# Performance work log

Hardware: AMD Instinct MI355X
Metric: run time of the kernel (lower is better)

Reference implementation:

```python
import jax, jax.numpy as jnp
import numpy as np

B, L, V, D = 8, 1024, 64, 64  # num_vars == d_model required by the module's g*h broadcast
EPS = 1e-5


def _layer_norm(x, gamma, beta):
    mu = jnp.mean(x, axis=-1, keepdims=True)
    var = jnp.mean(jnp.square(x - mu), axis=-1, keepdims=True)
    return (x - mu) * jax.lax.rsqrt(var + EPS) * gamma + beta


def setup_inputs() -> dict:
    key = jax.random.key(0)
    ks = jax.random.split(key, 20)
    s = 0.05
    inp = {
        'x': jax.random.normal(ks[0], (B, L, V), jnp.float32),
        # per-variable GRN(1, D, D) params, batched over V
        'W1': jax.random.normal(ks[1], (V, D), jnp.float32) * s,   # lin1 weight [in=1 -> D]
        'b1': jax.random.normal(ks[2], (V, D), jnp.float32) * s,
        'W2': jax.random.normal(ks[3], (V, D, D), jnp.float32) * s,
        'b2': jax.random.normal(ks[4], (V, D), jnp.float32) * s,
        'Wg': jax.random.normal(ks[5], (V, D, D), jnp.float32) * s,
        'bg': jax.random.normal(ks[6], (V, D), jnp.float32) * s,
        'Wsk': jax.random.normal(ks[7], (V, D), jnp.float32) * s,  # skip Linear(1, D)
        'bsk': jax.random.normal(ks[8], (V, D), jnp.float32) * s,
        'gamma': jnp.ones((V, D), jnp.float32),
        'beta': jnp.zeros((V, D), jnp.float32),
        # weight_net GRN(V*D, D, V) params
        'Wn1': jax.random.normal(ks[9], (V * D, D), jnp.float32) * s,
        'bn1': jax.random.normal(ks[10], (D,), jnp.float32) * s,
        'Wn2': jax.random.normal(ks[11], (D, D), jnp.float32) * s,
        'bn2': jax.random.normal(ks[12], (D,), jnp.float32) * s,
        'Wng': jax.random.normal(ks[13], (D, V), jnp.float32) * s,
        'bng': jax.random.normal(ks[14], (V,), jnp.float32) * s,
        'Wns': jax.random.normal(ks[15], (V * D, V), jnp.float32) * s,
        'bns': jax.random.normal(ks[16], (V,), jnp.float32) * s,
        'ngamma': jnp.ones((V,), jnp.float32),
        'nbeta': jnp.zeros((V,), jnp.float32),
    }
    return inp


def reference(x, W1, b1, W2, b2, Wg, bg, Wsk, bsk, gamma, beta,
              Wn1, bn1, Wn2, bn2, Wng, bng, Wns, bns, ngamma, nbeta):
    Bx, Lx, Vx = x.shape
    # --- per-variable GRN(1, D, D), batched over the variable axis ---
    h1 = jax.nn.elu(x[..., None] * W1 + b1)                      # [B,L,V,D]
    h2 = jnp.einsum('blvd,vde->blve', h1, W2) + b2               # [B,L,V,D]
    g = jax.nn.sigmoid(jnp.einsum('blvd,vde->blve', h2, Wg) + bg)
    skip = x[..., None] * Wsk + bsk                              # [B,L,V,D]
    stacked = _layer_norm(skip + g * h2, gamma, beta)            # [B,L,V,D]
    # --- weight net GRN(V*D, D, V) + softmax (note: requires V == D) ---
    flat = stacked.reshape(Bx, Lx, Vx * stacked.shape[-1])
    hw = jax.nn.elu(flat @ Wn1 + bn1)                            # [B,L,D]
    hw = hw @ Wn2 + bn2                                          # [B,L,D]
    gw = jax.nn.sigmoid(hw @ Wng + bng)                          # [B,L,V]
    skw = flat @ Wns + bns                                       # [B,L,V]
    weights = jax.nn.softmax(_layer_norm(skw + gw * hw, ngamma, nbeta), axis=-1)
    return jnp.einsum('blv,blvd->bld', weights, stacked)
```

## Files before the change

### kernel.cpp

```cpp
#include <hip/hip_runtime.h>
#include <hip/hip_bf16.h>
#include <math.h>

#define NV 64
#define ND 64
#define NTOK 8192
#define LN_EPS 1e-5f
#define SROW 4096
#define WROW 4096
#define KSPLIT 8
#define KR2 (4096 / KSPLIT)
#define BK 64
#define PROW2 (KSPLIT * 128)

typedef __attribute__((ext_vector_type(8))) short s8v;
typedef __attribute__((ext_vector_type(4))) float f4v;
typedef __attribute__((ext_vector_type(4))) int   i4v;

__device__ __forceinline__ float sigm_f(float x) {
    return __builtin_amdgcn_rcpf(1.f + __expf(-x));
}
__device__ __forceinline__ float elu_f(float x)  { return x > 0.f ? x : (__expf(x) - 1.f); }

__device__ __forceinline__ float bf16_to_f(unsigned short s) {
    union { unsigned int u; float f; } c; c.u = ((unsigned int)s) << 16;
    return c.f;
}
__device__ __forceinline__ unsigned short bf16_rn(float f) {
    union { float f; unsigned int u; } c; c.f = f;
    return (unsigned short)((c.u + 0x8000u) >> 16);
}

__global__ __launch_bounds__(256) void vsn_prepack(
    const float* __restrict__ W2, const float* __restrict__ Wg,
    const float* __restrict__ Wn1, const float* __restrict__ Wns,
    short* __restrict__ w2b, short* __restrict__ wgb,
    short* __restrict__ wct)
{
    __shared__ float T[64][65];
    const int b = blockIdx.x, t = threadIdx.x;

    if (b < 64) {
        const float* src = W2 + (size_t)b * 4096;
        short* dst = w2b + (size_t)b * 4096;
        #pragma unroll
        for (int pass = 0; pass < 2; ++pass) {
            #pragma unroll
            for (int i = 0; i < 16; ++i) {
                int id = i * 256 + t;
                T[id & 63][id >> 6] = src[id];
            }
            __syncthreads();
            #pragma unroll
            for (int i = 0; i < 16; ++i) {
                int id = i * 256 + t;
                dst[id] = (short)bf16_rn(T[id >> 6][id & 63]);
            }
            __syncthreads();
            src = Wg + (size_t)b * 4096;
            dst = wgb + (size_t)b * 4096;
        }
    } else {
        int tb = b - 64;
        int half = tb >> 6, kt = tb & 63;
        const float* src = (half == 0 ? Wn1 : Wns) + (size_t)(kt * 64) * 64;
        #pragma unroll
        for (int i = 0; i < 16; ++i) {
            int id = i * 256 + t;
            T[id & 63][id >> 6] = src[id];
        }
        __syncthreads();
        #pragma unroll
        for (int i = 0; i < 16; ++i) {
            int id = i * 256 + t;
            int n = id >> 6, r = id & 63;
            wct[(size_t)(half * 64 + n) * WROW + kt * 64 + r] = (short)bf16_rn(T[n][r]);
        }
    }
}

__global__ __launch_bounds__(256) void vsn_stage1(
    const float* __restrict__ x,
    const float* __restrict__ W1, const float* __restrict__ b1,
    const short* __restrict__ w2b, const short* __restrict__ wgb,
    const float* __restrict__ b2, const float* __restrict__ bg,
    const float* __restrict__ Wsk, const float* __restrict__ bsk,
    const float* __restrict__ gamma, const float* __restrict__ beta,
    unsigned short* __restrict__ stb)
{
    const int t = threadIdx.x;
    const int wave = t >> 6, lane = t & 63;
    const int m16 = lane & 15, quad = lane >> 4;
    const int v = blockIdx.y * 4 + wave;

    __shared__ float xs[4][32];
    __shared__ __align__(16) unsigned short h2s[4][32][72];

    float w1k[2][8], b1k[2][8];
    #pragma unroll
    for (int kt = 0; kt < 2; ++kt) {
        *(float4*)&w1k[kt][0] = *(const float4*)(W1 + v * 64 + kt * 32 + quad * 8);
        *(float4*)&w1k[kt][4] = *(const float4*)(W1 + v * 64 + kt * 32 + quad * 8 + 4);
        *(float4*)&b1k[kt][0] = *(const float4*)(b1 + v * 64 + kt * 32 + quad * 8);
        *(float4*)&b1k[kt][4] = *(const float4*)(b1 + v * 64 + kt * 32 + quad * 8 + 4);
    }
    float b2d[4], bgd[4], wskd[4], bskd[4], gamd[4], betd[4];
    #pragma unroll
    for (int ni = 0; ni < 4; ++ni) {
        int d = v * 64 + ni * 16 + m16;
        b2d[ni] = b2[d]; bgd[ni] = bg[d]; wskd[ni] = Wsk[d]; bskd[ni] = bsk[d];
        gamd[ni] = gamma[d]; betd[ni] = beta[d];
    }
    const size_t wb = (size_t)v * 4096;

    for (int tt4 = 0; tt4 < 4; ++tt4) {
        const int tile0 = blockIdx.x * 128 + tt4 * 32;

        if (lane < 32) xs[wave][lane] = x[(size_t)(tile0 + lane) * NV + v];

        s8v a[2][2];
        #pragma unroll
        for (int kt = 0; kt < 2; ++kt)
            #pragma unroll
            for (int mi = 0; mi < 2; ++mi) {
                float xv = xs[wave][mi * 16 + m16];
                float h[8];
                #pragma unroll
                for (int j = 0; j < 8; ++j) h[j] = elu_f(fmaf(xv, w1k[kt][j], b1k[kt][j]));
                i4v av;
                #pragma unroll
                for (int p = 0; p < 4; ++p) {
                    unsigned int u0 = __float_as_uint(h[2 * p]);
                    unsigned int u1 = __float_as_uint(h[2 * p + 1]);
                    av[p] = (int)((u1 & 0xffff0000u) | (u0 >> 16));
                }
                a[mi][kt] = *(s8v*)&av;
            }

        f4v hacc[2][4];
        #pragma unroll
        for (int mi = 0; mi < 2; ++mi)
            #pragma unroll
            for (int ni = 0; ni < 4; ++ni) hacc[mi][ni] = (f4v){0.f, 0.f, 0.f, 0.f};
        #pragma unroll
        for (int ni = 0; ni < 4; ++ni)
            #pragma unroll
            for (int kt = 0; kt < 2; ++kt) {
                s8v bh = *(const s8v*)(w2b + wb + (size_t)(ni * 16 + m16) * 64 + kt * 32 + quad * 8);
                #pragma unroll
                for (int mi = 0; mi < 2; ++mi)
                    hacc[mi][ni] = __builtin_amdgcn_mfma_f32_16x16x32_bf16(a[mi][kt], bh, hacc[mi][ni], 0, 0, 0);
            }
        #pragma unroll
        for (int mi = 0; mi < 2; ++mi)
            #pragma unroll
            for (int ni = 0; ni < 4; ++ni)
                #pragma unroll
                for (int r = 0; r < 4; ++r) hacc[mi][ni][r] += b2d[ni];

        #pragma unroll
        for (int mi = 0; mi < 2; ++mi)
            #pragma unroll
            for (int ni = 0; ni < 4; ++ni)
                #pragma unroll
                for (int r = 0; r < 4; ++r)
                    h2s[wave][mi * 16 + quad * 4 + r][ni * 16 + m16] =
                        (unsigned short)(__float_as_uint(hacc[mi][ni][r]) >> 16);

        s8v c[2][2];
        #pragma unroll
        for (int mi = 0; mi < 2; ++mi)
            #pragma unroll
            for (int kt = 0; kt < 2; ++kt)
                c[mi][kt] = *(const s8v*)&h2s[wave][mi * 16 + m16][kt * 32 + quad * 8];

        f4v gacc[2][4];
        #pragma unroll
        for (int mi = 0; mi < 2; ++mi)
            #pragma unroll
            for (int ni = 0; ni < 4; ++ni) gacc[mi][ni] = (f4v){0.f, 0.f, 0.f, 0.f};
        #pragma unroll
        for (int ni = 0; ni < 4; ++ni)
            #pragma unroll
            for (int kt = 0; kt < 2; ++kt) {
                s8v bh = *(const s8v*)(wgb + wb + (size_t)(ni * 16 + m16) * 64 + kt * 32 + quad * 8);
                #pragma unroll
                for (int mi = 0; mi < 2; ++mi)
                    gacc[mi][ni] = __builtin_amdgcn_mfma_f32_16x16x32_bf16(c[mi][kt], bh, gacc[mi][ni], 0, 0, 0);
            }

        {
            float xtok[2][4];
            #pragma unroll
            for (int mi = 0; mi < 2; ++mi)
                #pragma unroll
                for (int r = 0; r < 4; ++r) xtok[mi][r] = xs[wave][mi * 16 + quad * 4 + r];
            #pragma unroll
            for (int mi = 0; mi < 2; ++mi)
                #pragma unroll
                for (int ni = 0; ni < 4; ++ni)
                    #pragma unroll
                    for (int r = 0; r < 4; ++r) {
                        float g = sigm_f(gacc[mi][ni][r] + bgd[ni]);
                        gacc[mi][ni][r] = fmaf(xtok[mi][r], wskd[ni], bskd[ni]) + g * hacc[mi][ni][r];
                    }
        }

        #pragma unroll
        for (int mi = 0; mi < 2; ++mi)
            #pragma unroll
            for (int r = 0; r < 4; ++r) {
                float s0 = gacc[mi][0][r], s1 = gacc[mi][1][r], s2 = gacc[mi][2][r], s3 = gacc[mi][3][r];
                float sum = s0 + s1 + s2 + s3;
                float sq  = s0 * s0 + s1 * s1 + s2 * s2 + s3 * s3;
                #pragma unroll
                for (int m = 1; m < 16; m <<= 1) { sum += __shfl_xor(sum, m); sq += __shfl_xor(sq, m); }
                float mu  = sum * 0.015625f;
                float var = sq * 0.015625f - mu * mu;
                float rs  = __builtin_amdgcn_rsqf(var + LN_EPS);
                size_t base = (size_t)(tile0 + mi * 16 + quad * 4 + r) * SROW + (size_t)v * 64 + m16;
                #pragma unroll
                for (int ni = 0; ni < 4; ++ni)
                    stb[base + ni * 16] =
                        bf16_rn((gacc[mi][ni][r] - mu) * rs * gamd[ni] + betd[ni]);
            }
    }
}

__global__ __launch_bounds__(512) void vsn_stage2a(
    const unsigned short* __restrict__ stb,
    const short* __restrict__ wct,
    float* __restrict__ part)
{
    const int t = threadIdx.x;
    const int wave = t >> 6, lane = t & 63;
    const int m16 = lane & 15, quad = lane >> 4;
    const int mw = wave & 3, nw = wave >> 2;
    const int tok0 = blockIdx.x * 128;
    const int s = blockIdx.y;
    const int k0 = s * KR2;

    __shared__ __align__(16) unsigned short Al[128][72];
    __shared__ __align__(16) unsigned short Bl[128][72];

    const int srow = t >> 3;
    const int scol = (t & 7) * 8;
    const short* A = (const short*)stb;

    f4v acc[2][4];
    #pragma unroll
    for (int mi = 0; mi < 2; ++mi)
        #pragma unroll
        for (int nj = 0; nj < 4; ++nj) acc[mi][nj] = (f4v){0.f, 0.f, 0.f, 0.f};

    s8v pa[2], pb[2];
    #pragma unroll
    for (int q = 0; q < 2; ++q) {
        int row = srow + q * 64;
        pa[q] = *(const s8v*)(A + (size_t)(tok0 + row) * SROW + k0 + scol);
        pb[q] = *(const s8v*)(wct + (size_t)row * WROW + k0 + scol);
    }

    for (int kc = 0; kc < KR2 / BK; ++kc) {
        if (kc > 0) __syncthreads();
        #pragma unroll
        for (int q = 0; q < 2; ++q) {
            int row = srow + q * 64;
            *(s8v*)&Al[row][scol] = pa[q];
            *(s8v*)&Bl[row][scol] = pb[q];
        }
        __syncthreads();
        if (kc + 1 < KR2 / BK) {
            int kn = k0 + (kc + 1) * BK;
            #pragma unroll
            for (int q = 0; q < 2; ++q) {
                int row = srow + q * 64;
                pa[q] = *(const s8v*)(A + (size_t)(tok0 + row) * SROW + kn + scol);
                pb[q] = *(const s8v*)(wct + (size_t)row * WROW + kn + scol);
            }
        }
        #pragma unroll
        for (int ks = 0; ks < 2; ++ks) {
            s8v af[2], bf[4];
            #pragma unroll
            for (int mi = 0; mi < 2; ++mi)
                af[mi] = *(const s8v*)&Al[mw * 32 + mi * 16 + m16][ks * 32 + quad * 8];
            #pragma unroll
            for (int nj = 0; nj < 4; ++nj)
                bf[nj] = *(const s8v*)&Bl[nw * 64 + nj * 16 + m16][ks * 32 + quad * 8];
            #pragma unroll
            for (int mi = 0; mi < 2; ++mi)
                #pragma unroll
                for (int nj = 0; nj < 4; ++nj)
                    acc[mi][nj] = __builtin_amdgcn_mfma_f32_16x16x32_bf16(af[mi], bf[nj], acc[mi][nj], 0, 0, 0);
        }
    }

    #pragma unroll
    for (int mi = 0; mi < 2; ++mi)
        #pragma unroll
        for (int nj = 0; nj < 4; ++nj)
            #pragma unroll
            for (int r = 0; r < 4; ++r)
                part[(size_t)(tok0 + mw * 32 + mi * 16 + quad * 4 + r) * PROW2
                     + s * 128 + nw * 64 + nj * 16 + m16] = acc[mi][nj][r];
}

__global__ __launch_bounds__(256) void vsn_stage2b(
    const unsigned short* __restrict__ stb, const float* __restrict__ part,
    const float* __restrict__ bn1,
    const float* __restrict__ Wn2, const float* __restrict__ bn2,
    const float* __restrict__ Wng, const float* __restrict__ bng,
    const float* __restrict__ bns,
    const float* __restrict__ ngamma, const float* __restrict__ nbeta,
    float* __restrict__ out)
{
    const int t = threadIdx.x;
    const int tok0 = blockIdx.x * 8;
    const int lane = t & 63, wv = t >> 6;

    __shared__ __align__(16) float hw1_s[8][64];
    __shared__ __align__(16) float skw_s[8][64];
    __shared__ __align__(16) float hw2_s[8][64];
    __shared__ float s2_s[8][64];
    __shared__ float w_s[8][64];

    #pragma unroll
    for (int tk = 0; tk < 2; ++tk) {
        int tl = wv * 2 + tk;
        const float* pr = part + (size_t)(tok0 + tl) * PROW2
                        + (lane >> 5) * 128 + (lane & 31) * 4;
        float tv[4] = {0.f, 0.f, 0.f, 0.f};
        #pragma unroll
        for (int i = 0; i < 4; ++i) {
            float4 a = *(const float4*)(pr + i * 256);
            tv[0] += a.x; tv[1] += a.y; tv[2] += a.z; tv[3] += a.w;
        }
        #pragma unroll
        for (int c = 0; c < 4; ++c) tv[c] += __shfl_xor(tv[c], 32);
        if (lane < 16) {
            int j0 = lane * 4;
            float4 bb = *(const float4*)(bn1 + j0);
            hw1_s[tl][j0 + 0] = elu_f(tv[0] + bb.x);
            hw1_s[tl][j0 + 1] = elu_f(tv[1] + bb.y);
            hw1_s[tl][j0 + 2] = elu_f(tv[2] + bb.z);
            hw1_s[tl][j0 + 3] = elu_f(tv[3] + bb.w);
        } else if (lane < 32) {
            int j0 = (lane - 16) * 4;
            float4 bb = *(const float4*)(bns + j0);
            skw_s[tl][j0 + 0] = tv[0] + bb.x;
            skw_s[tl][j0 + 1] = tv[1] + bb.y;
            skw_s[tl][j0 + 2] = tv[2] + bb.z;
            skw_s[tl][j0 + 3] = tv[3] + bb.w;
        }
    }
    __syncthreads();

    #pragma unroll
    for (int i = 0; i < 2; ++i) {
        int oidx = i * 256 + t;
        int tt = oidx >> 6, jj = oidx & 63;
        float acc = bn2[jj];
        #pragma unroll
        for (int k4 = 0; k4 < 16; ++k4) {
            float4 h = *(const float4*)&hw1_s[tt][k4 * 4];
            acc += h.x * Wn2[(k4*4+0)*64+jj] + h.y * Wn2[(k4*4+1)*64+jj]
                 + h.z * Wn2[(k4*4+2)*64+jj] + h.w * Wn2[(k4*4+3)*64+jj];
        }
        hw2_s[tt][jj] = acc;
    }
    __syncthreads();

    #pragma unroll
    for (int i = 0; i < 2; ++i) {
        int oidx = i * 256 + t;
        int tt = oidx >> 6, vv = oidx & 63;
        float acc = bng[vv];
        #pragma unroll
        for (int k4 = 0; k4 < 16; ++k4) {
            float4 h = *(const float4*)&hw2_s[tt][k4 * 4];
            acc += h.x * Wng[(k4*4+0)*64+vv] + h.y * Wng[(k4*4+1)*64+vv]
                 + h.z * Wng[(k4*4+2)*64+vv] + h.w * Wng[(k4*4+3)*64+vv];
        }
        float gw = sigm_f(acc);
        s2_s[tt][vv] = skw_s[tt][vv] + gw * hw2_s[tt][vv];
    }
    __syncthreads();

    const int vloc = lane >> 3, d8 = (lane & 7) * 8;
    s8v r0[8], r1[8];
    {
        const short* s0 = (const short*)stb + (size_t)(tok0 + wv * 2) * SROW + d8;
        const short* s1 = s0 + SROW;
        #pragma unroll
        for (int vc = 0; vc < 8; ++vc) {
            r0[vc] = *(const s8v*)(s0 + (vc * 8 + vloc) * 64);
            r1[vc] = *(const s8v*)(s1 + (vc * 8 + vloc) * 64);
        }
    }

    if (t < 128) {
        int tt = t >> 4, l = t & 15;
        float z[4]; float sum = 0.f, sq = 0.f;
        #pragma unroll
        for (int i = 0; i < 4; ++i) { z[i] = s2_s[tt][l + 16 * i]; sum += z[i]; sq += z[i] * z[i]; }
        #pragma unroll
        for (int m = 1; m < 16; m <<= 1) { sum += __shfl_xor(sum, m); sq += __shfl_xor(sq, m); }
        float mu  = sum * 0.015625f;
        float var = sq * 0.015625f - mu * mu;
        float rs  = __builtin_amdgcn_rsqf(var + LN_EPS);
        float ln[4]; float mx = -1e30f;
        #pragma unroll
        for (int i = 0; i < 4; ++i) {
            ln[i] = (z[i] - mu) * rs * ngamma[l + 16 * i] + nbeta[l + 16 * i];
            mx = fmaxf(mx, ln[i]);
        }
        #pragma unroll
        for (int m = 1; m < 16; m <<= 1) mx = fmaxf(mx, __shfl_xor(mx, m));
        float es = 0.f; float ev[4];
        #pragma unroll
        for (int i = 0; i < 4; ++i) { ev[i] = __expf(ln[i] - mx); es += ev[i]; }
        #pragma unroll
        for (int m = 1; m < 16; m <<= 1) es += __shfl_xor(es, m);
        float inv = __builtin_amdgcn_rcpf(es);
        #pragma unroll
        for (int i = 0; i < 4; ++i) w_s[tt][l + 16 * i] = ev[i] * inv;
    }
    __syncthreads();

    {
        float acc0[8], acc1[8];
        #pragma unroll
        for (int j = 0; j < 8; ++j) { acc0[j] = 0.f; acc1[j] = 0.f; }
        #pragma unroll
        for (int vc = 0; vc < 8; ++vc) {
            int v = vc * 8 + vloc;
            float w0 = w_s[wv * 2][v], w1 = w_s[wv * 2 + 1][v];
            #pragma unroll
            for (int j = 0; j < 8; ++j) {
                acc0[j] = fmaf(w0, bf16_to_f((unsigned short)r0[vc][j]), acc0[j]);
                acc1[j] = fmaf(w1, bf16_to_f((unsigned short)r1[vc][j]), acc1[j]);
            }
        }
        #pragma unroll
        for (int m = 8; m <= 32; m <<= 1)
            #pragma unroll
            for (int j = 0; j < 8; ++j) {
                acc0[j] += __shfl_xor(acc0[j], m);
                acc1[j] += __shfl_xor(acc1[j], m);
            }
        if (lane < 8) {
            float* op = out + (size_t)(tok0 + wv * 2) * 64 + lane * 8;
            *(float4*)op       = make_float4(acc0[0], acc0[1], acc0[2], acc0[3]);
            *(float4*)(op + 4) = make_float4(acc0[4], acc0[5], acc0[6], acc0[7]);
            op += 64;
            *(float4*)op       = make_float4(acc1[0], acc1[1], acc1[2], acc1[3]);
            *(float4*)(op + 4) = make_float4(acc1[4], acc1[5], acc1[6], acc1[7]);
        }
    }
}

extern "C" void kernel_launch(void* const* d_in, const int* in_sizes, int n_in,
                              void* d_out, int out_size, void* d_ws, size_t ws_size,
                              hipStream_t stream) {
    const float* x     = (const float*)d_in[0];
    const float* W1    = (const float*)d_in[1];
    const float* b1    = (const float*)d_in[2];
    const float* W2    = (const float*)d_in[3];
    const float* b2    = (const float*)d_in[4];
    const float* Wg    = (const float*)d_in[5];
    const float* bg    = (const float*)d_in[6];
    const float* Wsk   = (const float*)d_in[7];
    const float* bsk   = (const float*)d_in[8];
    const float* gamma = (const float*)d_in[9];
    const float* beta  = (const float*)d_in[10];
    const float* Wn1   = (const float*)d_in[11];
    const float* bn1   = (const float*)d_in[12];
    const float* Wn2   = (const float*)d_in[13];
    const float* bn2   = (const float*)d_in[14];
    const float* Wng   = (const float*)d_in[15];
    const float* bng   = (const float*)d_in[16];
    const float* Wns   = (const float*)d_in[17];
    const float* bns   = (const float*)d_in[18];
    const float* ngam  = (const float*)d_in[19];
    const float* nbet  = (const float*)d_in[20];

    char* ws = (char*)d_ws;
    unsigned short* stb = (unsigned short*)ws;
    short* wct = (short*)(ws + (64u << 20));
    short* w2b = (short*)(ws + (65u << 20));
    short* wgb = w2b + 262144;
    float* part = (float*)(ws + (66u << 20));
    float* outp = (float*)d_out;

    vsn_prepack<<<dim3(192), 256, 0, stream>>>(W2, Wg, Wn1, Wns, w2b, wgb, wct);
    vsn_stage1<<<dim3(NTOK / 128, 16), 256, 0, stream>>>(
        x, W1, b1, w2b, wgb, b2, bg, Wsk, bsk, gamma, beta, stb);
    vsn_stage2a<<<dim3(NTOK / 128, KSPLIT), 512, 0, stream>>>(stb, wct, part);
    vsn_stage2b<<<dim3(NTOK / 8), 256, 0, stream>>>(
        stb, part, bn1, Wn2, bn2, Wng, bng, bns, ngam, nbet, outp);
}
```

Before: 186.3 us.

## Transpose stage1 MFMA orientation for packed stores; async LDS loads with swizzle in stage2a

Stage1 swaps the MFMA operand roles so each lane holds four consecutive feature values per token. This turns the scalar bf16 stores of the normalized output and the h2 staging writes into packed 64-bit stores, and moves the per-feature params into shared memory. Stage2a replaces register-staged loads with global_load_lds async copies into double-buffered, XOR-swizzled LDS tiles. That removes padding and register staging in exchange for relying on the direct-to-LDS load path and its lane-to-address mapping being correct.

```diff
diff --git a/kernel.cpp b/kernel.cpp
--- a/kernel.cpp
+++ b/kernel.cpp
@@ -11,6 +11,7 @@
 #define KSPLIT 8
 #define KR2 (4096 / KSPLIT)
 #define BK 64
+#define NKC (KR2 / BK)
 #define PROW2 (KSPLIT * 128)
 
 typedef __attribute__((ext_vector_type(8))) short s8v;
@@ -29,6 +30,18 @@
 __device__ __forceinline__ unsigned short bf16_rn(float f) {
     union { float f; unsigned int u; } c; c.f = f;
     return (unsigned short)((c.u + 0x8000u) >> 16);
+}
+__device__ __forceinline__ unsigned int pk2rn(float a, float b) {
+    return (unsigned int)bf16_rn(a) | ((unsigned int)bf16_rn(b) << 16);
+}
+__device__ __forceinline__ unsigned int pk2t(float a, float b) {
+    return (__float_as_uint(a) >> 16) | (__float_as_uint(b) & 0xffff0000u);
+}
+__device__ __forceinline__ void async16(const void* g, void* l) {
+    __builtin_amdgcn_global_load_lds(
+        (const __attribute__((address_space(1))) unsigned int*)g,
+        (__attribute__((address_space(3))) unsigned int*)l,
+        16, 0, 0);
 }
 
 __global__ __launch_bounds__(256) void vsn_prepack(
@@ -93,8 +106,18 @@
     const int m16 = lane & 15, quad = lane >> 4;
     const int v = blockIdx.y * 4 + wave;
 
-    __shared__ float xs[4][32];
     __shared__ __align__(16) unsigned short h2s[4][32][72];
+    __shared__ __align__(16) float pl[4][6][64];
+
+    {
+        int dd = lane;
+        pl[wave][0][dd] = b2[v * 64 + dd];
+        pl[wave][1][dd] = bg[v * 64 + dd];
+        pl[wave][2][dd] = Wsk[v * 64 + dd];
+        pl[wave][3][dd] = bsk[v * 64 + dd];
+        pl[wave][4][dd] = gamma[v * 64 + dd];
+        pl[wave][5][dd] = beta[v * 64 + dd];
+    }
 
     float w1k[2][8], b1k[2][8];
     #pragma unroll
@@ -104,126 +127,131 @@
         *(float4*)&b1k[kt][0] = *(const float4*)(b1 + v * 64 + kt * 32 + quad * 8);
         *(float4*)&b1k[kt][4] = *(const float4*)(b1 + v * 64 + kt * 32 + quad * 8 + 4);
     }
-    float b2d[4], bgd[4], wskd[4], bskd[4], gamd[4], betd[4];
-    #pragma unroll
-    for (int ni = 0; ni < 4; ++ni) {
-        int d = v * 64 + ni * 16 + m16;
-        b2d[ni] = b2[d]; bgd[ni] = bg[d]; wskd[ni] = Wsk[d]; bskd[ni] = bsk[d];
-        gamd[ni] = gamma[d]; betd[ni] = beta[d];
-    }
     const size_t wb = (size_t)v * 4096;
 
     for (int tt4 = 0; tt4 < 4; ++tt4) {
         const int tile0 = blockIdx.x * 128 + tt4 * 32;
 
-        if (lane < 32) xs[wave][lane] = x[(size_t)(tile0 + lane) * NV + v];
-
-        s8v a[2][2];
+        float xld = x[(size_t)(tile0 + (lane & 31)) * NV + v];
+        float xv[2];
+        xv[0] = __shfl(xld, m16);
+        xv[1] = __shfl(xld, 16 + m16);
+
+        s8v bh1[2][2];
+        #pragma unroll
+        for (int ti = 0; ti < 2; ++ti)
+            #pragma unroll
+            for (int kt = 0; kt < 2; ++kt) {
+                float h[8];
+                #pragma unroll
+                for (int j = 0; j < 8; ++j) h[j] = elu_f(fmaf(xv[ti], w1k[kt][j], b1k[kt][j]));
+                i4v av;
+                #pragma unroll
+                for (int p = 0; p < 4; ++p)
+                    av[p] = (int)pk2t(h[2 * p], h[2 * p + 1]);
+                bh1[ti][kt] = *(s8v*)&av;
+            }
+
+        f4v hacc[4][2];
+        #pragma unroll
+        for (int ei = 0; ei < 4; ++ei)
+            #pragma unroll
+            for (int ti = 0; ti < 2; ++ti) hacc[ei][ti] = (f4v){0.f, 0.f, 0.f, 0.f};
         #pragma unroll
         for (int kt = 0; kt < 2; ++kt)
             #pragma unroll
-            for (int mi = 0; mi < 2; ++mi) {
-                float xv = xs[wave][mi * 16 + m16];
-                float h[8];
-                #pragma unroll
-                for (int j = 0; j < 8; ++j) h[j] = elu_f(fmaf(xv, w1k[kt][j], b1k[kt][j]));
-                i4v av;
-                #pragma unroll
-                for (int p = 0; p < 4; ++p) {
-                    unsigned int u0 = __float_as_uint(h[2 * p]);
-                    unsigned int u1 = __float_as_uint(h[2 * p + 1]);
-                    av[p] = (int)((u1 & 0xffff0000u) | (u0 >> 16));
+            for (int ei = 0; ei < 4; ++ei) {
+                s8v aw = *(const s8v*)(w2b + wb + (size_t)(ei * 16 + m16) * 64 + kt * 32 + quad * 8);
+                #pragma unroll
+                for (int ti = 0; ti < 2; ++ti)
+                    hacc[ei][ti] = __builtin_amdgcn_mfma_f32_16x16x32_bf16(aw, bh1[ti][kt], hacc[ei][ti], 0, 0, 0);
+            }
+
+        #pragma unroll
+        for (int ei = 0; ei < 4; ++ei) {
+            float bq[4];
+            *(float4*)bq = *(const float4*)&pl[wave][0][ei * 16 + quad * 4];
+            #pragma unroll
+            for (int ti = 0; ti < 2; ++ti) {
+                #pragma unroll
+                for (int r = 0; r < 4; ++r) hacc[ei][ti][r] += bq[r];
+                uint2 pk = make_uint2(pk2t(hacc[ei][ti][0], hacc[ei][ti][1]),
+                                      pk2t(hacc[ei][ti][2], hacc[ei][ti][3]));
+                *(uint2*)&h2s[wave][ti * 16 + m16][ei * 16 + quad * 4] = pk;
+            }
+        }
+
+        s8v bh2[2][2];
+        #pragma unroll
+        for (int ti = 0; ti < 2; ++ti)
+            #pragma unroll
+            for (int kt = 0; kt < 2; ++kt)
+                bh2[ti][kt] = *(const s8v*)&h2s[wave][ti * 16 + m16][kt * 32 + quad * 8];
+
+        f4v gacc[4][2];
+        #pragma unroll
+        for (int ei = 0; ei < 4; ++ei)
+            #pragma unroll
+            for (int ti = 0; ti < 2; ++ti) gacc[ei][ti] = (f4v){0.f, 0.f, 0.f, 0.f};
+        #pragma unroll
+        for (int kt = 0; kt < 2; ++kt)
+            #pragma unroll
+            for (int ei = 0; ei < 4; ++ei) {
+                s8v ag = *(const s8v*)(wgb + wb + (size_t)(ei * 16 + m16) * 64 + kt * 32 + quad * 8);
+                #pragma unroll
+                for (int ti = 0; ti < 2; ++ti)
+                    gacc[ei][ti] = __builtin_amdgcn_mfma_f32_16x16x32_bf16(ag, bh2[ti][kt], gacc[ei][ti], 0, 0, 0);
+            }
+
+        #pragma unroll
+        for (int ei = 0; ei < 4; ++ei) {
+            float bgq[4], wkq[4], bkq[4];
+            *(float4*)bgq = *(const float4*)&pl[wave][1][ei * 16 + quad * 4];
+            *(float4*)wkq = *(const float4*)&pl[wave][2][ei * 16 + quad * 4];
+            *(float4*)bkq = *(const float4*)&pl[wave][3][ei * 16 + quad * 4];
+            #pragma unroll
+            for (int ti = 0; ti < 2; ++ti)
+                #pragma unroll
+                for (int r = 0; r < 4; ++r) {
+                    float g = sigm_f(gacc[ei][ti][r] + bgq[r]);
+                    gacc[ei][ti][r] = fmaf(xv[ti], wkq[r], bkq[r]) + g * hacc[ei][ti][r];
                 }
-                a[mi][kt] = *(s8v*)&av;
-            }
-
-        f4v hacc[2][4];
-        #pragma unroll
-        for (int mi = 0; mi < 2; ++mi)
-            #pragma unroll
-            for (int ni = 0; ni < 4; ++ni) hacc[mi][ni] = (f4v){0.f, 0.f, 0.f, 0.f};
-        #pragma unroll
-        for (int ni = 0; ni < 4; ++ni)
-            #pragma unroll
-            for (int kt = 0; kt < 2; ++kt) {
-                s8v bh = *(const s8v*)(w2b + wb + (size_t)(ni * 16 + m16) * 64 + kt * 32 + quad * 8);
-                #pragma unroll
-                for (int mi = 0; mi < 2; ++mi)
-                    hacc[mi][ni] = __builtin_amdgcn_mfma_f32_16x16x32_bf16(a[mi][kt], bh, hacc[mi][ni], 0, 0, 0);
-            }
-        #pragma unroll
-        for (int mi = 0; mi < 2; ++mi)
-            #pragma unroll
-            for (int ni = 0; ni < 4; ++ni)
-                #pragma unroll
-                for (int r = 0; r < 4; ++r) hacc[mi][ni][r] += b2d[ni];
-
-        #pragma unroll
-        for (int mi = 0; mi < 2; ++mi)
-            #pragma unroll
-            for (int ni = 0; ni < 4; ++ni)
-                #pragma unroll
-                for (int r = 0; r < 4; ++r)
-                    h2s[wave][mi * 16 + quad * 4 + r][ni * 16 + m16] =
-                        (unsigned short)(__float_as_uint(hacc[mi][ni][r]) >> 16);
-
-        s8v c[2][2];
-        #pragma unroll
-        for (int mi = 0; mi < 2; ++mi)
-            #pragma unroll
-            for (int kt = 0; kt < 2; ++kt)
-                c[mi][kt] = *(const s8v*)&h2s[wave][mi * 16 + m16][kt * 32 + quad * 8];
-
-        f4v gacc[2][4];
-        #pragma unroll
-        for (int mi = 0; mi < 2; ++mi)
-            #pragma unroll
-            for (int ni = 0; ni < 4; ++ni) gacc[mi][ni] = (f4v){0.f, 0.f, 0.f, 0.f};
-        #pragma unroll
-        for (int ni = 0; ni < 4; ++ni)
-            #pragma unroll
-            for (int kt = 0; kt < 2; ++kt) {
-                s8v bh = *(const s8v*)(wgb + wb + (size_t)(ni * 16 + m16) * 64 + kt * 32 + quad * 8);
-                #pragma unroll
-                for (int mi = 0; mi < 2; ++mi)
-                    gacc[mi][ni] = __builtin_amdgcn_mfma_f32_16x16x32_bf16(c[mi][kt], bh, gacc[mi][ni], 0, 0, 0);
-            }
-
-        {
-            float xtok[2][4];
-            #pragma unroll
-            for (int mi = 0; mi < 2; ++mi)
-                #pragma unroll
-                for (int r = 0; r < 4; ++r) xtok[mi][r] = xs[wave][mi * 16 + quad * 4 + r];
-            #pragma unroll
-            for (int mi = 0; mi < 2; ++mi)
-                #pragma unroll
-                for (int ni = 0; ni < 4; ++ni)
-                    #pragma unroll
-                    for (int r = 0; r < 4; ++r) {
-                        float g = sigm_f(gacc[mi][ni][r] + bgd[ni]);
-                        gacc[mi][ni][r] = fmaf(xtok[mi][r], wskd[ni], bskd[ni]) + g * hacc[mi][ni][r];
-                    }
-        }
-
-        #pragma unroll
-        for (int mi = 0; mi < 2; ++mi)
-            #pragma unroll
-            for (int r = 0; r < 4; ++r) {
-                float s0 = gacc[mi][0][r], s1 = gacc[mi][1][r], s2 = gacc[mi][2][r], s3 = gacc[mi][3][r];
-                float sum = s0 + s1 + s2 + s3;
-                float sq  = s0 * s0 + s1 * s1 + s2 * s2 + s3 * s3;
-                #pragma unroll
-                for (int m = 1; m < 16; m <<= 1) { sum += __shfl_xor(sum, m); sq += __shfl_xor(sq, m); }
-                float mu  = sum * 0.015625f;
-                float var = sq * 0.015625f - mu * mu;
-                float rs  = __builtin_amdgcn_rsqf(var + LN_EPS);
-                size_t base = (size_t)(tile0 + mi * 16 + quad * 4 + r) * SROW + (size_t)v * 64 + m16;
-                #pragma unroll
-                for (int ni = 0; ni < 4; ++ni)
-                    stb[base + ni * 16] =
-                        bf16_rn((gacc[mi][ni][r] - mu) * rs * gamd[ni] + betd[ni]);
-            }
+        }
+
+        float mu[2], rs[2];
+        #pragma unroll
+        for (int ti = 0; ti < 2; ++ti) {
+            float sum = 0.f, sq = 0.f;
+            #pragma unroll
+            for (int ei = 0; ei < 4; ++ei)
+                #pragma unroll
+                for (int r = 0; r < 4; ++r) {
+                    float z = gacc[ei][ti][r];
+                    sum += z; sq = fmaf(z, z, sq);
+                }
+            sum += __shfl_xor(sum, 16); sq += __shfl_xor(sq, 16);
+            sum += __shfl_xor(sum, 32); sq += __shfl_xor(sq, 32);
+            mu[ti] = sum * 0.015625f;
+            float var = sq * 0.015625f - mu[ti] * mu[ti];
+            rs[ti] = __builtin_amdgcn_rsqf(var + LN_EPS);
+        }
+
+        #pragma unroll
+        for (int ei = 0; ei < 4; ++ei) {
+            float gq[4], bq[4];
+            *(float4*)gq = *(const float4*)&pl[wave][4][ei * 16 + quad * 4];
+            *(float4*)bq = *(const float4*)&pl[wave][5][ei * 16 + quad * 4];
+            #pragma unroll
+            for (int ti = 0; ti < 2; ++ti) {
+                float n0 = (gacc[ei][ti][0] - mu[ti]) * rs[ti] * gq[0] + bq[0];
+                float n1 = (gacc[ei][ti][1] - mu[ti]) * rs[ti] * gq[1] + bq[1];
+                float n2 = (gacc[ei][ti][2] - mu[ti]) * rs[ti] * gq[2] + bq[2];
+                float n3 = (gacc[ei][ti][3] - mu[ti]) * rs[ti] * gq[3] + bq[3];
+                uint2 pk = make_uint2(pk2rn(n0, n1), pk2rn(n2, n3));
+                *(uint2*)(stb + (size_t)(tile0 + ti * 16 + m16) * SROW
+                          + v * 64 + ei * 16 + quad * 4) = pk;
+            }
+        }
     }
 }
 
@@ -240,12 +268,11 @@
     const int s = blockIdx.y;
     const int k0 = s * KR2;
 
-    __shared__ __align__(16) unsigned short Al[128][72];
-    __shared__ __align__(16) unsigned short Bl[128][72];
+    __shared__ __align__(16) unsigned short Al[2][128 * 64];
+    __shared__ __align__(16) unsigned short Bl[2][128 * 64];
 
     const int srow = t >> 3;
-    const int scol = (t & 7) * 8;
-    const short* A = (const short*)stb;
+    const int schunk = t & 7;
 
     f4v acc[2][4];
     #pragma unroll
@@ -253,47 +280,47 @@
         #pragma unroll
         for (int nj = 0; nj < 4; ++nj) acc[mi][nj] = (f4v){0.f, 0.f, 0.f, 0.f};
 
-    s8v pa[2], pb[2];
-    #pragma unroll
-    for (int q = 0; q < 2; ++q) {
-        int row = srow + q * 64;
-        pa[q] = *(const s8v*)(A + (size_t)(tok0 + row) * SROW + k0 + scol);
-        pb[q] = *(const s8v*)(wct + (size_t)row * WROW + k0 + scol);
-    }
-
-    for (int kc = 0; kc < KR2 / BK; ++kc) {
-        if (kc > 0) __syncthreads();
+    auto STAGE = [&](int buf, int kc) {
+        const int kb = k0 + kc * BK;
         #pragma unroll
         for (int q = 0; q < 2; ++q) {
-            int row = srow + q * 64;
-            *(s8v*)&Al[row][scol] = pa[q];
-            *(s8v*)&Bl[row][scol] = pb[q];
+            const int row = srow + q * 64;
+            const int sc = (schunk ^ (row & 7)) * 8;
+            async16(stb + (size_t)(tok0 + row) * SROW + kb + sc,
+                    &Al[buf][q * 4096 + wave * 512]);
+            async16(wct + (size_t)row * WROW + kb + sc,
+                    &Bl[buf][q * 4096 + wave * 512]);
+        }
+    };
+
+    STAGE(0, 0);
+    __syncthreads();
+
+    for (int kc = 0; kc < NKC; ++kc) {
+        const int buf = kc & 1;
+        if (kc + 1 < NKC) STAGE(buf ^ 1, kc + 1);
+        #pragma unroll
+        for (int ks = 0; ks < 2; ++ks) {
+            s8v af[2], bfr[4];
+            #pragma unroll
+            for (int mi = 0; mi < 2; ++mi) {
+                int row = mw * 32 + mi * 16 + m16;
+                int ch = ((ks * 4 + quad) ^ (row & 7)) * 8;
+                af[mi] = *(const s8v*)&Al[buf][row * 64 + ch];
+            }
+            #pragma unroll
+            for (int nj = 0; nj < 4; ++nj) {
+                int row = nw * 64 + nj * 16 + m16;
+                int ch = ((ks * 4 + quad) ^ (row & 7)) * 8;
+                bfr[nj] = *(const s8v*)&Bl[buf][row * 64 + ch];
+            }
+            #pragma unroll
+            for (int mi = 0; mi < 2; ++mi)
+                #pragma unroll
+                for (int nj = 0; nj < 4; ++nj)
+                    acc[mi][nj] = __builtin_amdgcn_mfma_f32_16x16x32_bf16(af[mi], bfr[nj], acc[mi][nj], 0, 0, 0);
         }
         __syncthreads();
-        if (kc + 1 < KR2 / BK) {
-            int kn = k0 + (kc + 1) * BK;
-            #pragma unroll
-            for (int q = 0; q < 2; ++q) {
-                int row = srow + q * 64;
-                pa[q] = *(const s8v*)(A + (size_t)(tok0 + row) * SROW + kn + scol);
-                pb[q] = *(const s8v*)(wct + (size_t)row * WROW + kn + scol);
-            }
-        }
-        #pragma unroll
-        for (int ks = 0; ks < 2; ++ks) {
-            s8v af[2], bf[4];
-            #pragma unroll
-            for (int mi = 0; mi < 2; ++mi)
-                af[mi] = *(const s8v*)&Al[mw * 32 + mi * 16 + m16][ks * 32 + quad * 8];
-            #pragma unroll
-            for (int nj = 0; nj < 4; ++nj)
-                bf[nj] = *(const s8v*)&Bl[nw * 64 + nj * 16 + m16][ks * 32 + quad * 8];
-            #pragma unroll
-            for (int mi = 0; mi < 2; ++mi)
-                #pragma unroll
-                for (int nj = 0; nj < 4; ++nj)
-                    acc[mi][nj] = __builtin_amdgcn_mfma_f32_16x16x32_bf16(af[mi], bf[nj], acc[mi][nj], 0, 0, 0);
-        }
     }
 
     #pragma unroll
```

New measurement: 196.2 us. +5.3%, slower.

## Restructure stage2a GEMM with async global-to-LDS double buffering and XOR swizzle

Applied to the files above, without the earlier changes.

Rewrites the split-K GEMM over the flattened stacked activations so it fills shared memory with direct global-to-LDS async loads into double buffers, using an XOR-swizzled layout to avoid bank conflicts. The tile shrinks to 64 tokens with 256 threads, and the K split drops from 8 to 4, which halves the partial-sum buffer traffic and the reduction work in stage2b. The aim is to hide load latency and cut register staging, at the cost of fewer K-parallel blocks and longer per-block K loops.

```diff
diff --git a/kernel.cpp b/kernel.cpp
--- a/kernel.cpp
+++ b/kernel.cpp
@@ -8,9 +8,11 @@
 #define LN_EPS 1e-5f
 #define SROW 4096
 #define WROW 4096
-#define KSPLIT 8
+#define KSPLIT 4
 #define KR2 (4096 / KSPLIT)
 #define BK 64
+#define NKC (KR2 / BK)
+#define MT2 64
 #define PROW2 (KSPLIT * 128)
 
 typedef __attribute__((ext_vector_type(8))) short s8v;
@@ -29,6 +31,12 @@
 __device__ __forceinline__ unsigned short bf16_rn(float f) {
     union { float f; unsigned int u; } c; c.f = f;
     return (unsigned short)((c.u + 0x8000u) >> 16);
+}
+__device__ __forceinline__ void async16(const void* g, void* l) {
+    __builtin_amdgcn_global_load_lds(
+        (const __attribute__((address_space(1))) unsigned int*)g,
+        (__attribute__((address_space(3))) unsigned int*)l,
+        16, 0, 0);
 }
 
 __global__ __launch_bounds__(256) void vsn_prepack(
@@ -227,7 +235,7 @@
     }
 }
 
-__global__ __launch_bounds__(512) void vsn_stage2a(
+__global__ __launch_bounds__(256) void vsn_stage2a(
     const unsigned short* __restrict__ stb,
     const short* __restrict__ wct,
     float* __restrict__ part)
@@ -235,75 +243,76 @@
     const int t = threadIdx.x;
     const int wave = t >> 6, lane = t & 63;
     const int m16 = lane & 15, quad = lane >> 4;
-    const int mw = wave & 3, nw = wave >> 2;
-    const int tok0 = blockIdx.x * 128;
+    const int nw = wave;
+    const int tok0 = blockIdx.x * MT2;
     const int s = blockIdx.y;
     const int k0 = s * KR2;
 
-    __shared__ __align__(16) unsigned short Al[128][72];
-    __shared__ __align__(16) unsigned short Bl[128][72];
-
-    const int srow = t >> 3;
-    const int scol = (t & 7) * 8;
-    const short* A = (const short*)stb;
-
-    f4v acc[2][4];
-    #pragma unroll
-    for (int mi = 0; mi < 2; ++mi)
-        #pragma unroll
-        for (int nj = 0; nj < 4; ++nj) acc[mi][nj] = (f4v){0.f, 0.f, 0.f, 0.f};
-
-    s8v pa[2], pb[2];
-    #pragma unroll
-    for (int q = 0; q < 2; ++q) {
-        int row = srow + q * 64;
-        pa[q] = *(const s8v*)(A + (size_t)(tok0 + row) * SROW + k0 + scol);
-        pb[q] = *(const s8v*)(wct + (size_t)row * WROW + k0 + scol);
-    }
-
-    for (int kc = 0; kc < KR2 / BK; ++kc) {
-        if (kc > 0) __syncthreads();
+    __shared__ __align__(16) unsigned short Al[2][64 * 64];
+    __shared__ __align__(16) unsigned short Bl[2][128 * 64];
+
+    f4v acc[4][2];
+    #pragma unroll
+    for (int mi = 0; mi < 4; ++mi)
+        #pragma unroll
+        for (int nj = 0; nj < 2; ++nj) acc[mi][nj] = (f4v){0.f, 0.f, 0.f, 0.f};
+
+    auto STAGE = [&](int buf, int kc) {
+        const int kb = k0 + kc * BK;
         #pragma unroll
         for (int q = 0; q < 2; ++q) {
-            int row = srow + q * 64;
-            *(s8v*)&Al[row][scol] = pa[q];
-            *(s8v*)&Bl[row][scol] = pb[q];
+            const int row = wave * 16 + q * 8 + (lane >> 3);
+            const int sc = ((lane & 7) ^ (row & 7)) * 8;
+            async16(stb + (size_t)(tok0 + row) * SROW + kb + sc,
+                    &Al[buf][wave * 1024 + q * 512]);
+        }
+        #pragma unroll
+        for (int q = 0; q < 4; ++q) {
+            const int row = wave * 32 + q * 8 + (lane >> 3);
+            const int sc = ((lane & 7) ^ (row & 7)) * 8;
+            async16(wct + (size_t)row * WROW + kb + sc,
+                    &Bl[buf][wave * 2048 + q * 512]);
+        }
+    };
+
+    STAGE(0, 0);
+    __syncthreads();
+
+    for (int kc = 0; kc < NKC; ++kc) {
+        const int buf = kc & 1;
+        if (kc + 1 < NKC) STAGE(buf ^ 1, kc + 1);
+        #pragma unroll
+        for (int ks = 0; ks < 2; ++ks) {
+            s8v af[4], bfr[2];
+            #pragma unroll
+            for (int mi = 0; mi < 4; ++mi) {
+                int row = mi * 16 + m16;
+                int ch = ((ks * 4 + quad) ^ (row & 7)) * 8;
+                af[mi] = *(const s8v*)&Al[buf][row * 64 + ch];
+            }
+            #pragma unroll
+            for (int nj = 0; nj < 2; ++nj) {
+                int row = nw * 32 + nj * 16 + m16;
+                int ch = ((ks * 4 + quad) ^ (row & 7)) * 8;
+                bfr[nj] = *(const s8v*)&Bl[buf][row * 64 + ch];
+            }
+            #pragma unroll
+            for (int mi = 0; mi < 4; ++mi)
+                #pragma unroll
+                for (int nj = 0; nj < 2; ++nj)
+                    acc[mi][nj] = __builtin_amdgcn_mfma_f32_16x16x32_bf16(af[mi], bfr[nj], acc[mi][nj], 0, 0, 0);
         }
         __syncthreads();
-        if (kc + 1 < KR2 / BK) {
-            int kn = k0 + (kc + 1) * BK;
-            #pragma unroll
-            for (int q = 0; q < 2; ++q) {
-                int row = srow + q * 64;
-                pa[q] = *(const s8v*)(A + (size_t)(tok0 + row) * SROW + kn + scol);
-                pb[q] = *(const s8v*)(wct + (size_t)row * WROW + kn + scol);
-            }
-        }
-        #pragma unroll
-        for (int ks = 0; ks < 2; ++ks) {
-            s8v af[2], bf[4];
-            #pragma unroll
-            for (int mi = 0; mi < 2; ++mi)
-                af[mi] = *(const s8v*)&Al[mw * 32 + mi * 16 + m16][ks * 32 + quad * 8];
-            #pragma unroll
-            for (int nj = 0; nj < 4; ++nj)
-                bf[nj] = *(const s8v*)&Bl[nw * 64 + nj * 16 + m16][ks * 32 + quad * 8];
-            #pragma unroll
-            for (int mi = 0; mi < 2; ++mi)
-                #pragma unroll
-                for (int nj = 0; nj < 4; ++nj)
-                    acc[mi][nj] = __builtin_amdgcn_mfma_f32_16x16x32_bf16(af[mi], bf[nj], acc[mi][nj], 0, 0, 0);
-        }
-    }
-
-    #pragma unroll
-    for (int mi = 0; mi < 2; ++mi)
-        #pragma unroll
-        for (int nj = 0; nj < 4; ++nj)
+    }
+
+    #pragma unroll
+    for (int mi = 0; mi < 4; ++mi)
+        #pragma unroll
+        for (int nj = 0; nj < 2; ++nj)
             #pragma unroll
             for (int r = 0; r < 4; ++r)
-                part[(size_t)(tok0 + mw * 32 + mi * 16 + quad * 4 + r) * PROW2
-                     + s * 128 + nw * 64 + nj * 16 + m16] = acc[mi][nj][r];
+                part[(size_t)(tok0 + mi * 16 + quad * 4 + r) * PROW2
+                     + s * 128 + nw * 32 + nj * 16 + m16] = acc[mi][nj][r];
 }
 
 __global__ __launch_bounds__(256) void vsn_stage2b(
@@ -332,7 +341,7 @@
                         + (lane >> 5) * 128 + (lane & 31) * 4;
         float tv[4] = {0.f, 0.f, 0.f, 0.f};
         #pragma unroll
-        for (int i = 0; i < 4; ++i) {
+        for (int i = 0; i < 2; ++i) {
             float4 a = *(const float4*)(pr + i * 256);
             tv[0] += a.x; tv[1] += a.y; tv[2] += a.z; tv[3] += a.w;
         }
@@ -496,7 +505,7 @@
     vsn_prepack<<<dim3(192), 256, 0, stream>>>(W2, Wg, Wn1, Wns, w2b, wgb, wct);
     vsn_stage1<<<dim3(NTOK / 128, 16), 256, 0, stream>>>(
         x, W1, b1, w2b, wgb, b2, bg, Wsk, bsk, gamma, beta, stb);
-    vsn_stage2a<<<dim3(NTOK / 128, KSPLIT), 512, 0, stream>>>(stb, wct, part);
+    vsn_stage2a<<<dim3(NTOK / MT2, KSPLIT), 256, 0, stream>>>(stb, wct, part);
     vsn_stage2b<<<dim3(NTOK / 8), 256, 0, stream>>>(
         stb, part, bn1, Wn2, bn2, Wng, bng, bns, ngam, nbet, outp);
 }
```

After: 190.4 us. +2.2%, slower.

## Use async global-to-LDS loads with double buffering and XOR swizzle in stage2a

Applied to the files above, without the earlier changes.

Stage2a now loads its A and B tiles straight from global memory into LDS with global_load_lds, replacing the register staging step. Two LDS buffers let the load for chunk k+2 run while chunk k is being computed. Column chunks are XOR-swizzled in place of the padded rows to avoid LDS bank conflicts. The cost is hand-placed waitcnt and barrier calls whose correctness depends on exact vmcnt counting, and twice the LDS per block, which may lower occupancy.

```diff
diff --git a/kernel.cpp b/kernel.cpp
--- a/kernel.cpp
+++ b/kernel.cpp
@@ -11,6 +11,7 @@
 #define KSPLIT 8
 #define KR2 (4096 / KSPLIT)
 #define BK 64
+#define NKC (KR2 / BK)
 #define PROW2 (KSPLIT * 128)
 
 typedef __attribute__((ext_vector_type(8))) short s8v;
@@ -29,6 +30,12 @@
 __device__ __forceinline__ unsigned short bf16_rn(float f) {
     union { float f; unsigned int u; } c; c.f = f;
     return (unsigned short)((c.u + 0x8000u) >> 16);
+}
+__device__ __forceinline__ void async16(const void* g, void* l) {
+    __builtin_amdgcn_global_load_lds(
+        (const __attribute__((address_space(1))) unsigned int*)g,
+        (__attribute__((address_space(3))) unsigned int*)l,
+        16, 0, 0);
 }
 
 __global__ __launch_bounds__(256) void vsn_prepack(
@@ -240,12 +247,11 @@
     const int s = blockIdx.y;
     const int k0 = s * KR2;
 
-    __shared__ __align__(16) unsigned short Al[128][72];
-    __shared__ __align__(16) unsigned short Bl[128][72];
+    __shared__ __align__(16) unsigned short Al[2][128 * 64];
+    __shared__ __align__(16) unsigned short Bl[2][128 * 64];
 
     const int srow = t >> 3;
-    const int scol = (t & 7) * 8;
-    const short* A = (const short*)stb;
+    const int schunk = t & 7;
 
     f4v acc[2][4];
     #pragma unroll
@@ -253,47 +259,55 @@
         #pragma unroll
         for (int nj = 0; nj < 4; ++nj) acc[mi][nj] = (f4v){0.f, 0.f, 0.f, 0.f};
 
-    s8v pa[2], pb[2];
-    #pragma unroll
-    for (int q = 0; q < 2; ++q) {
-        int row = srow + q * 64;
-        pa[q] = *(const s8v*)(A + (size_t)(tok0 + row) * SROW + k0 + scol);
-        pb[q] = *(const s8v*)(wct + (size_t)row * WROW + k0 + scol);
-    }
-
-    for (int kc = 0; kc < KR2 / BK; ++kc) {
-        if (kc > 0) __syncthreads();
+    auto STAGE = [&](int buf, int kc) {
+        const int kb = k0 + kc * BK;
         #pragma unroll
         for (int q = 0; q < 2; ++q) {
-            int row = srow + q * 64;
-            *(s8v*)&Al[row][scol] = pa[q];
-            *(s8v*)&Bl[row][scol] = pb[q];
-        }
-        __syncthreads();
-        if (kc + 1 < KR2 / BK) {
-            int kn = k0 + (kc + 1) * BK;
-            #pragma unroll
-            for (int q = 0; q < 2; ++q) {
-                int row = srow + q * 64;
-                pa[q] = *(const s8v*)(A + (size_t)(tok0 + row) * SROW + kn + scol);
-                pb[q] = *(const s8v*)(wct + (size_t)row * WROW + kn + scol);
-            }
-        }
+            const int row = srow + q * 64;
+            const int sc = (schunk ^ (row & 7)) * 8;
+            async16(stb + (size_t)(tok0 + row) * SROW + kb + sc,
+                    &Al[buf][q * 4096 + wave * 512]);
+            async16(wct + (size_t)row * WROW + kb + sc,
+                    &Bl[buf][q * 4096 + wave * 512]);
+        }
+    };
+
+    STAGE(0, 0);
+    STAGE(1, 1);
+
+    for (int kc = 0; kc < NKC; ++kc) {
+        const int buf = kc & 1;
+        if (kc + 1 < NKC) asm volatile("s_waitcnt vmcnt(4)" ::: "memory");
+        else              asm volatile("s_waitcnt vmcnt(0)" ::: "memory");
+        __builtin_amdgcn_s_barrier();
+        __builtin_amdgcn_sched_barrier(0);
+
         #pragma unroll
         for (int ks = 0; ks < 2; ++ks) {
-            s8v af[2], bf[4];
+            s8v af[2], bfr[4];
+            #pragma unroll
+            for (int mi = 0; mi < 2; ++mi) {
+                int row = mw * 32 + mi * 16 + m16;
+                int ch = ((ks * 4 + quad) ^ (row & 7)) * 8;
+                af[mi] = *(const s8v*)&Al[buf][row * 64 + ch];
+            }
+            #pragma unroll
+            for (int nj = 0; nj < 4; ++nj) {
+                int row = nw * 64 + nj * 16 + m16;
+                int ch = ((ks * 4 + quad) ^ (row & 7)) * 8;
+                bfr[nj] = *(const s8v*)&Bl[buf][row * 64 + ch];
+            }
             #pragma unroll
             for (int mi = 0; mi < 2; ++mi)
-                af[mi] = *(const s8v*)&Al[mw * 32 + mi * 16 + m16][ks * 32 + quad * 8];
-            #pragma unroll
-            for (int nj = 0; nj < 4; ++nj)
-                bf[nj] = *(const s8v*)&Bl[nw * 64 + nj * 16 + m16][ks * 32 + quad * 8];
-            #pragma unroll
-            for (int mi = 0; mi < 2; ++mi)
                 #pragma unroll
                 for (int nj = 0; nj < 4; ++nj)
-                    acc[mi][nj] = __builtin_amdgcn_mfma_f32_16x16x32_bf16(af[mi], bf[nj], acc[mi][nj], 0, 0, 0);
-        }
+                    acc[mi][nj] = __builtin_amdgcn_mfma_f32_16x16x32_bf16(af[mi], bfr[nj], acc[mi][nj], 0, 0, 0);
+        }
+
+        asm volatile("s_waitcnt lgkmcnt(0)" ::: "memory");
+        __builtin_amdgcn_s_barrier();
+        __builtin_amdgcn_sched_barrier(0);
+        if (kc + 2 < NKC) STAGE(buf, kc + 2);
     }
 
     #pragma unroll
```

New measurement: 185.5 us, median of 2. No clear change (-0.4%).
